# Kernel tuning notes

Measured on AMD Instinct MI355X. Metric: run time of the kernel, lower is better.

The kernel has to match this reference:

```python
import jax, jax.numpy as jnp
import numpy as np

N, E = 8000, 96000
S, V, G = 128, 64, 64          # scalar channels, l=1 vector channels, gate channels
LAT, OH = 128, 64
D = S + 3 * V                  # 320 feature dim per node/edge
AVG_NEIGH = 12.0
EPS = 1e-8

def _split(x):
    return x[:, :S], x[:, S:].reshape(x.shape[0], V, 3)

def sep_layernorm(x, ws, bs, wv):
    # separable LN: layernorm on l=0 scalars, component RMS norm on l=1 vectors
    s, v = _split(x)
    mu = jnp.mean(s, -1, keepdims=True)
    sc = s - mu
    s = sc * jax.lax.rsqrt(jnp.mean(sc * sc, -1, keepdims=True) + EPS) * ws + bs
    v = v * jax.lax.rsqrt(jnp.mean(v * v, (-2, -1), keepdims=True) + EPS) * wv[:, None]
    return s, v

def edge_frame(ev):
    # orthonormal frame with first axis along the edge (SO2 m=0 axis)
    a = ev * jax.lax.rsqrt(jnp.sum(ev * ev, -1, keepdims=True) + EPS)
    ref = jnp.where(jnp.abs(a[:, :1]) < 0.9,
                    jnp.array([1.0, 0.0, 0.0], ev.dtype),
                    jnp.array([0.0, 1.0, 0.0], ev.dtype))
    b = jnp.cross(a, ref)
    b = b * jax.lax.rsqrt(jnp.sum(b * b, -1, keepdims=True) + EPS)
    c = jnp.cross(a, b)
    return jnp.stack([a, b, c], axis=1)  # [E,3,3], rows are frame axes

def gate_act(s_all, v, n_s, n_g):
    s, g = s_all[:, :n_s], s_all[:, n_s:n_s + n_g]
    return jax.nn.silu(s), jax.nn.sigmoid(g)[:, :, None] * v

def e3_linear(s, v, ws, bs, wv):
    s = s @ ws * (1.0 / np.sqrt(s.shape[-1])) + bs
    v = jnp.einsum('eum,uk->ekm', v, wv) * (1.0 / np.sqrt(v.shape[1]))
    return s, v

def setup_inputs() -> dict:
    key = jax.random.key(0)
    ks = jax.random.split(key, 20)
    f = jnp.float32
    p = lambda k, sh: jax.random.normal(k, sh, f)
    inp = {}
    inp['latents'] = p(ks[0], (E, LAT))
    inp['node_features'] = p(ks[1], (N, D))
    inp['edge_features'] = p(ks[2], (E, D))
    at = jax.random.randint(ks[3], (N,), 0, OH)
    inp['atom_type'] = at
    inp['node_onehot'] = jax.nn.one_hot(at, OH, dtype=f)
    inp['edge_index'] = jax.random.randint(ks[4], (2, E), 0, N)
    inp['edge_vector'] = p(ks[5], (E, 3))
    inp['active_edges'] = jnp.arange(E)
    inp['sln_n_ws'] = jnp.ones((S,), f); inp['sln_n_bs'] = jnp.zeros((S,), f); inp['sln_n_wv'] = jnp.ones((V,), f)
    inp['sln_e_ws'] = jnp.ones((S,), f); inp['sln_e_bs'] = jnp.zeros((S,), f); inp['sln_e_wv'] = jnp.ones((V,), f)
    inp['so2_w0'] = p(ks[6], (3 * S + 3 * V, S + G + V))
    inp['so2_w1r'] = p(ks[7], (3 * V, V))
    inp['so2_w1i'] = p(ks[8], (3 * V, V))
    inp['env_w'] = p(ks[9], (LAT, S + V))
    inp['lp_ws'] = p(ks[10], (S, S)); inp['lp_bs'] = jnp.zeros((S,), f); inp['lp_wv'] = p(ks[11], (V, V))
    inp['oh_w_ss'] = p(ks[12], (S, OH, S))
    inp['oh_w_sg'] = p(ks[13], (S, OH, G))
    inp['oh_w_vv'] = p(ks[14], (V, OH, V))
    inp['ohl_ws'] = p(ks[15], (S, S)); inp['ohl_bs'] = jnp.zeros((S,), f); inp['ohl_wv'] = p(ks[16], (V, V))
    inp['res_param'] = jnp.zeros((1,), f)
    return inp

def reference(latents, node_features, edge_features, atom_type, node_onehot,
              edge_index, edge_vector, active_edges,
              sln_n_ws, sln_n_bs, sln_n_wv, sln_e_ws, sln_e_bs, sln_e_wv,
              so2_w0, so2_w1r, so2_w1i, env_w,
              lp_ws, lp_bs, lp_wv,
              oh_w_ss, oh_w_sg, oh_w_vv, ohl_ws, ohl_bs, ohl_wv, res_param):
    ctr = edge_index[0][active_edges]
    nbr = edge_index[1][active_edges]
    ns, nv = sep_layernorm(node_features, sln_n_ws, sln_n_bs, sln_n_wv)
    es, evf = sep_layernorm(edge_features, sln_e_ws, sln_e_bs, sln_e_wv)
    # concat center | edge | neighbor (scalars and vectors kept separate)
    sc = jnp.concatenate([ns[ctr], es, ns[nbr]], -1)          # [E, 3S]
    vc = jnp.concatenate([nv[ctr], evf, nv[nbr]], 1)          # [E, 3V, 3]
    R = edge_frame(edge_vector[active_edges])
    vf = jnp.einsum('eij,euj->eui', R, vc)                    # rotate into edge frame
    # SO2 linear: m=0 mixes scalars + on-axis components; m=+-1 mix with (re,im) weights
    m0_in = jnp.concatenate([sc, vf[:, :, 0]], -1)            # [E, 3S+3V]
    m0_out = m0_in @ so2_w0 * (1.0 / np.sqrt(m0_in.shape[-1]))  # [E, S+G+V]
    n1 = 1.0 / np.sqrt(vf.shape[1])
    vp = (vf[:, :, 1] @ so2_w1r - vf[:, :, 2] @ so2_w1i) * n1
    vm = (vf[:, :, 1] @ so2_w1i + vf[:, :, 2] @ so2_w1r) * n1
    v_out = jnp.stack([m0_out[:, S + G:], vp, vm], -1)        # [E,V,3] in frame
    v_out = jnp.einsum('eij,eui->euj', R, v_out)              # rotate back
    # gate activation + post linear
    ms, mv = gate_act(m0_out[:, :S + G], v_out, S, G)
    ms, mv = e3_linear(ms, mv, lp_ws, lp_bs, lp_wv)
    # env weighting (E3ElementLinear with weights from latents) + scatter to centers
    w = latents[active_edges] @ env_w * (1.0 / np.sqrt(LAT))  # [E, S+V]
    ms = ms * w[:, :S]
    mv = mv * w[:, S:, None]
    inv = 1.0 / np.sqrt(AVG_NEIGH)
    agg_s = jax.ops.segment_sum(ms, ctr, num_segments=N) * inv
    agg_v = jax.ops.segment_sum(mv, ctr, num_segments=N) * inv
    # one-hot FullyConnectedTensorProduct -> gate -> linear
    n_ss = 1.0 / np.sqrt(S * OH)
    n_vv = 1.0 / np.sqrt(V * OH)
    t_s = jnp.einsum('nu,nv,uvk->nk', agg_s, node_onehot, oh_w_ss) * n_ss
    t_g = jnp.einsum('nu,nv,uvk->nk', agg_s, node_onehot, oh_w_sg) * n_ss
    t_v = jnp.einsum('num,nv,uvk->nkm', agg_v, node_onehot, oh_w_vv) * n_vv
    gs, gv = gate_act(jnp.concatenate([t_s, t_g], -1), t_v, S, G)
    os_, ov = e3_linear(gs, gv, ohl_ws, ohl_bs, ohl_wv)
    new = jnp.concatenate([os_, ov.reshape(-1, 3 * V)], -1)
    # residual mixing (identity residual since node_irreps_in == irreps_out)
    alpha = jax.nn.sigmoid(res_param)[0]
    return alpha * node_features + (1.0 - alpha) * new
```

## Files before the change

### kernel.cpp

```cpp
#include <hip/hip_runtime.h>

#define EPS_LN 1e-8f

typedef __bf16 bf16x8 __attribute__((ext_vector_type(8)));
typedef float  f32x4  __attribute__((ext_vector_type(4)));

__device__ __forceinline__ float sigmoidf_(float x){ return 1.0f/(1.0f+__expf(-x)); }
__device__ __forceinline__ float siluf_(float x){ return x*sigmoidf_(x); }
__device__ __forceinline__ unsigned short f2bf(float x){ union{ __bf16 b; unsigned short u;} c; c.b = (__bf16)x; return c.u; }
__device__ __forceinline__ float bf2f(unsigned short u){ return __uint_as_float(((unsigned)u)<<16); }

union F4 { float4 v; float f[4]; };

__device__ __forceinline__ void st_bf4(char* base, int row, int stride_bytes, int k,
                                       float x0, float x1, float x2, float x3){
    union { __bf16 h[4]; unsigned long long u; } p;
    p.h[0]=(__bf16)x0; p.h[1]=(__bf16)x1; p.h[2]=(__bf16)x2; p.h[3]=(__bf16)x3;
    *(unsigned long long*)(base + row*stride_bytes + ((2*k) ^ ((row&7)<<4))) = p.u;
}
__device__ __forceinline__ bf16x8 ld_frag(const char* base, int row, int stride_bytes, int kbyte){
    return *(const bf16x8*)(base + row*stride_bytes + (kbyte ^ ((row&7)<<4)));
}
__device__ __forceinline__ void st_g4(__bf16* p, float x0, float x1, float x2, float x3){
    union { __bf16 h[4]; unsigned long long u; } pk;
// ... 26 lines not shown
                         const float* __restrict__ oh_vv,
                         __bf16* __restrict__ Wt, __bf16* __restrict__ w1rt, __bf16* __restrict__ w1it,
                         __bf16* __restrict__ Wevfm, __bf16* __restrict__ Bnodefm,
                         __bf16* __restrict__ Bvfm,
                         __bf16* __restrict__ envfm, __bf16* __restrict__ lpsfm,
                         __bf16* __restrict__ lpvfm,
                         __bf16* __restrict__ ssT, __bf16* __restrict__ sgT, __bf16* __restrict__ vvT)
{
    int t = blockIdx.x*256 + threadIdx.x;
    if (t < 576*256){
        int n = t/576, k = t%576;
        Wt[t] = (__bf16)w0[(size_t)k*256 + n];
    }
    if (t < 256*320){
        int n = t/320, k = t%320;
        int src = (k<128) ? (128+k) : (384+(k-128));
        Wevfm[fm_idx(n,k,10)] = (__bf16)w0[(size_t)src*256 + n];
    }
    if (t < 512*128){
        int n = t/128, k = t%128;
        float v = (n<256) ? w0[(size_t)k*256 + n] : w0[(size_t)(256+k)*256 + (n-256)];
        Bnodefm[fm_idx(n,k,4)] = (__bf16)v;
    }
    if (t < 64*192){
        int c = t/192, k = t%192;
        w1rt[t] = (__bf16)w1r[(size_t)k*64 + c];
        w1it[t] = (__bf16)w1i[(size_t)k*64 + c];
    }
    if (t < 128*384){
        int n = t/384, k = t%384;
        float v;
        if (n < 64) v = (k<192) ? w1r[(size_t)k*64+n] : -w1i[(size_t)(k-192)*64+n];
        else        v = (k<192) ? w1i[(size_t)k*64+(n-64)] : w1r[(size_t)(k-192)*64+(n-64)];
        Bvfm[fm_idx(n,k,12)] = (__bf16)v;
    }
    if (t < 192*128){ int n=t/128, k=t%128; envfm[fm_idx(n,k,4)] = (__bf16)env_w[(size_t)k*192+n]; }
    if (t < 128*128){ int n=t/128, k=t%128; lpsfm[fm_idx(n,k,4)] = (__bf16)lp_ws[(size_t)k*128+n]; }
    if (t < 64*64)  { int n=t/64,  k=t%64;  lpvfm[fm_idx(n,k,2)] = (__bf16)lp_wv[(size_t)k*64+n]; }
    if (t < 64*128*128){
        int at = t / 16384; int r = t & 16383; int u = r >> 7, k = r & 127;
        ssT[t] = (__bf16)oh_ss[((size_t)u*64 + at)*128 + k];
    }
    if (t < 64*128*64){
        int at = t / 8192; int r = t & 8191; int u = r >> 6, k = r & 63;
        sgT[t] = (__bf16)oh_sg[((size_t)u*64 + at)*64 + k];
    }
    if (t < 64*64*64){
        int at = t / 4096; int r = t & 4095; int u = r >> 6, k = r & 63;
        vvT[t] = (__bf16)oh_vv[((size_t)u*64 + at)*64 + k];
    }
}

__global__ void csr_count(const int* __restrict__ ei, const int* __restrict__ act,
                          int* __restrict__ cnt, int EA)
{
    int e = blockIdx.x*256 + threadIdx.x;
    if (e < EA) atomicAdd(&cnt[ei[act[e]]], 1);
}
__global__ void csr_scan(const int* __restrict__ cnt, int* __restrict__ offs,
                         int* __restrict__ cursor, int N)
{
    __shared__ int part[256];
    int t = threadIdx.x;
    int chunk = (N + 255) / 256;
    int lo = t*chunk, hi = lo+chunk; if (hi > N) hi = N; if (lo > N) lo = N;
    int s = 0;
    for (int i=lo;i<hi;i++) s += cnt[i];
    part[t] = s;
    __syncthreads();
    for (int d=1; d<256; d<<=1){
        int v = (t>=d) ? part[t-d] : 0;
        __syncthreads();
        part[t] += v;
        __syncthreads();
    }
    int run = (t==0) ? 0 : part[t-1];
    for (int i=lo;i<hi;i++){
        offs[i] = run; cursor[i] = run;
        run += cnt[i];
    }
    if (t==255) offs[N] = part[255];
}
__global__ void csr_fill(const int* __restrict__ ei, const int* __restrict__ act,
                         int* __restrict__ cursor, int* __restrict__ elist, int EA)
{
    int e = blockIdx.x*256 + threadIdx.x;
    if (e < EA){
        int n = ei[act[e]];
        int p = atomicAdd(&cursor[n], 1);
        elist[p] = e;
    }
}

__global__ void node_ln_kernel(const float* __restrict__ nf,
                               const float* __restrict__ ws, const float* __restrict__ bs,
                               const float* __restrict__ wv,
                               float* __restrict__ ns, float* __restrict__ nv,
                               __bf16* __restrict__ nsb, __bf16* __restrict__ nvb, int N)
{
    int t = threadIdx.x;
    int lane = t & 63;
    int n = blockIdx.x*4 + (t>>6);
    if (n >= N) return;
    const float* row = nf + (size_t)n*320;
    float s0 = row[lane], s1 = row[64+lane];
    float sum = s0+s1, sq = s0*s0+s1*s1;
    #pragma unroll
    for (int m=1;m<64;m<<=1){ sum += __shfl_xor(sum,m,64); sq += __shfl_xor(sq,m,64); }
    float mu = sum*(1.0f/128.0f);
    float rs = rsqrtf(sq*(1.0f/128.0f) - mu*mu + EPS_LN);
    float o0 = (s0-mu)*rs*ws[lane]    + bs[lane];
    float o1 = (s1-mu)*rs*ws[64+lane] + bs[64+lane];
    ns[(size_t)n*128+lane]    = o0;
    ns[(size_t)n*128+64+lane] = o1;
    nsb[(size_t)n*128+lane]    = (__bf16)o0;
    nsb[(size_t)n*128+64+lane] = (__bf16)o1;
    float v0 = row[128+lane], v1 = row[192+lane], v2 = row[256+lane];
    float vs = v0*v0+v1*v1+v2*v2;
    #pragma unroll
    for (int m=1;m<64;m<<=1) vs += __shfl_xor(vs,m,64);
    float rv = rsqrtf(vs*(1.0f/192.0f) + EPS_LN);
    float nv0 = v0*rv*wv[lane/3];
    float nv1 = v1*rv*wv[(64+lane)/3];
    float nv2 = v2*rv*wv[(128+lane)/3];
    nv[(size_t)n*192+lane]     = nv0;
    nv[(size_t)n*192+64+lane]  = nv1;
    nv[(size_t)n*192+128+lane] = nv2;
    nvb[(size_t)n*192+lane]     = (__bf16)nv0;
    nvb[(size_t)n*192+64+lane]  = (__bf16)nv1;
    nvb[(size_t)n*192+128+lane] = (__bf16)nv2;
}

__global__ void stage_kernel(
    const float* __restrict__ ef_all,
    const int*   __restrict__ edge_index,
    const float* __restrict__ edge_vector,
    const int*   __restrict__ active_edges,
    const float* __restrict__ e_ws, const float* __restrict__ e_bs, const float* __restrict__ e_wv,
    const __bf16* __restrict__ nvb,
    __bf16* __restrict__ m0in,
    __bf16* __restrict__ vfg,
    float* __restrict__ Rg, int2* __restrict__ ctnb,
    int EA, int EF)
{
    int tid = blockIdx.x*256 + threadIdx.x;
    int e = tid >> 4, l = tid & 15;
    if (e >= EA) return;
    int ae = active_edges[e];
    int ct = edge_index[ae];
    int nb = edge_index[EF + ae];
    float ex = edge_vector[(size_t)ae*3+0];
    float ey = edge_vector[(size_t)ae*3+1];
    float ez = edge_vector[(size_t)ae*3+2];
    float rn = rsqrtf(ex*ex+ey*ey+ez*ez + EPS_LN);
    float ax = ex*rn, ay = ey*rn, az = ez*rn;
    float rx, ry;
    if (fabsf(ax) < 0.9f) { rx = 1.0f; ry = 0.0f; } else { rx = 0.0f; ry = 1.0f; }
    float bx = -az*ry, by = az*rx, bz = ax*ry - ay*rx;
    float bn = rsqrtf(bx*bx+by*by+bz*bz + EPS_LN);
    bx*=bn; by*=bn; bz*=bn;
    float cx = ay*bz - az*by;
    float cy = az*bx - ax*bz;
    float cz = ax*by - ay*bx;
    if (l == 0){
        float* Rr = Rg + (size_t)e*12;
        *(float4*)(Rr)   = make_float4(ax,ay,az,bx);
        *(float4*)(Rr+4) = make_float4(by,bz,cx,cy);
        *(float4*)(Rr+8) = make_float4(cz,0.f,0.f,0.f);
        ctnb[e] = make_int2(ct, nb);
    }
    __bf16* Arow = m0in + (size_t)e*320;
    __bf16* V1r  = vfg + (size_t)e*384;
    __bf16* V2r  = V1r + 192;
    const float* ef = ef_all + (size_t)e*320;
    {
        F4 sa, sb;
        sa.v = *(const float4*)(ef + l*4);
        sb.v = *(const float4*)(ef + 64 + l*4);
        float sum=0.f, sq=0.f;
        #pragma unroll
        for (int i=0;i<4;i++){ sum += sa.f[i]+sb.f[i]; sq += sa.f[i]*sa.f[i]+sb.f[i]*sb.f[i]; }
        #pragma unroll
        for (int m=1;m<16;m<<=1){ sum += __shfl_xor(sum,m,64); sq += __shfl_xor(sq,m,64); }
        float mu = sum*(1.0f/128.0f);
        float rs = rsqrtf(sq*(1.0f/128.0f)-mu*mu + EPS_LN);
        float o0[4], o1[4];
        #pragma unroll
        for (int i=0;i<4;i++){
            int c0 = l*4+i, c1 = 64+l*4+i;
            o0[i] = (sa.f[i]-mu)*rs*e_ws[c0]+e_bs[c0];
            o1[i] = (sb.f[i]-mu)*rs*e_ws[c1]+e_bs[c1];
        }
        st_g4(Arow + l*4,      o0[0],o0[1],o0[2],o0[3]);
        st_g4(Arow + 64 + l*4, o1[0],o1[1],o1[2],o1[3]);
    }
    {
        F4 va, vb, vc;
        va.v = *(const float4*)(ef + 128 + l*12);
        vb.v = *(const float4*)(ef + 128 + l*12 + 4);
        vc.v = *(const float4*)(ef + 128 + l*12 + 8);
        float vv[12];
        #pragma unroll
        for (int i=0;i<4;i++){ vv[i]=va.f[i]; vv[4+i]=vb.f[i]; vv[8+i]=vc.f[i]; }
        float sq=0.f;
        #pragma unroll
        for (int i=0;i<12;i++) sq += vv[i]*vv[i];
        #pragma unroll
        for (int m=1;m<16;m<<=1) sq += __shfl_xor(sq,m,64);
        float rv = rsqrtf(sq*(1.0f/192.0f) + EPS_LN);
        float f0[4], f1[4], f2[4];
        #pragma unroll
        for (int j=0;j<4;j++){
            int u = 4*l + j;
            float sc = rv * e_wv[u];
            float x = vv[3*j]*sc, y = vv[3*j+1]*sc, z = vv[3*j+2]*sc;
            f0[j] = ax*x+ay*y+az*z;
            f1[j] = bx*x+by*y+bz*z;
            f2[j] = cx*x+cy*y+cz*z;
        }
        st_g4(Arow + 128 + 64 + 4*l, f0[0],f0[1],f0[2],f0[3]);
        st_g4(V1r + 64 + 4*l, f1[0],f1[1],f1[2],f1[3]);
        st_g4(V2r + 64 + 4*l, f2[0],f2[1],f2[2],f2[3]);
    }
    {
        float vv[12];
        ld_bf12(nvb + (size_t)ct*192 + l*12, vv);
        float f0[4], f1[4], f2[4];
        #pragma unroll
        for (int j=0;j<4;j++){
            float x = vv[3*j], y = vv[3*j+1], z = vv[3*j+2];
            f0[j] = ax*x+ay*y+az*z;
            f1[j] = bx*x+by*y+bz*z;
            f2[j] = cx*x+cy*y+cz*z;
        }
        st_g4(Arow + 128 + 4*l, f0[0],f0[1],f0[2],f0[3]);
        st_g4(V1r + 4*l, f1[0],f1[1],f1[2],f1[3]);
        st_g4(V2r + 4*l, f2[0],f2[1],f2[2],f2[3]);
    }
    {
        float vv[12];
        ld_bf12(nvb + (size_t)nb*192 + l*12, vv);
        float f0[4], f1[4], f2[4];
        #pragma unroll
        for (int j=0;j<4;j++){
            float x = vv[3*j], y = vv[3*j+1], z = vv[3*j+2];
            f0[j] = ax*x+ay*y+az*z;
            f1[j] = bx*x+by*y+bz*z;
            f2[j] = cx*x+cy*y+cz*z;
        }
        st_g4(Arow + 128 + 128 + 4*l, f0[0],f0[1],f0[2],f0[3]);
        st_g4(V1r + 128 + 4*l, f1[0],f1[1],f1[2],f1[3]);
        st_g4(V2r + 128 + 4*l, f2[0],f2[1],f2[2],f2[3]);
    }
}

enum { EPI_PLAIN=0, EPI_LPS=1, EPI_LPV=2 };

template<int N, int K, int RT, int EPI, bool AGATHER>
__global__ __launch_bounds__((N/64)*RT*64)
void gemm_k(const __bf16* __restrict__ Ag, const float* __restrict__ Agf,
            const int* __restrict__ aidx,
            const __bf16* __restrict__ Bfm,
            unsigned short* __restrict__ outp,
            const unsigned short* __restrict__ wenv,
            const float* __restrict__ bias,
            float scale, int M)
{
    constexpr int NT  = N/64;
    constexpr int BM  = RT*64;
    constexpr int T   = NT*RT*64;
    constexpr int NKT = K/32;
    constexpr int NK  = K/64;
    constexpr int NBUF= (NK>1) ? 2 : 1;
    constexpr int CA  = (BM*8 + T - 1)/T;
    __shared__ __align__(16) char lA[NBUF][BM*128];

    const int tid  = threadIdx.x;
    const int brow = blockIdx.x*BM;
    const int mpl  = blockIdx.y;
    const __bf16* A = AGATHER ? nullptr : (Ag + (size_t)mpl*M*K);

    uint4 ra[CA];
    auto loadA = [&](int ks){
        #pragma unroll
        for (int i=0;i<CA;i++){
            int c = tid + i*T;
            if (c < BM*8){
                int r = c>>3;
                int gr = brow + r; if (gr >= M) gr = M-1;
                if constexpr (AGATHER){
                    int ae = aidx[gr];
                    const float* base = Agf + (size_t)ae*K + ks*64 + (c&7)*8;
                    float4 f0 = *(const float4*)(base);
                    float4 f1 = *(const float4*)(base+4);
                    ra[i] = pack8(f0, f1);
                } else {
                    ra[i] = *(const uint4*)((const char*)(A + (size_t)gr*K + ks*64) + (c&7)*16);
                }
            }
        }
    };
    auto storeA = [&](int buf){
        #pragma unroll
        for (int i=0;i<CA;i++){
            int c = tid + i*T;
            if (c < BM*8){
                int r = c>>3, off = (c&7)*16;
                *(uint4*)(&lA[buf][r*128 + (off ^ ((r&7)<<4))]) = ra[i];
            }
        }
    };

    const int wid = tid>>6, ln = tid&63;
    const int cc = ln & 15, gq = ln >> 4;
    const int wn = wid % NT, wm = wid / NT;
    const __bf16* bbase = Bfm + ((size_t)wn*4*NKT)*512 + (size_t)ln*8;

    f32x4 acc[4][4];
    #pragma unroll
    for (int i=0;i<4;i++)
        #pragma unroll
        for (int j=0;j<4;j++) acc[i][j] = (f32x4){0,0,0,0};

    loadA(0); storeA(0);
    int cur = 0;
    for (int ks=0; ks<NK; ks++){
        __syncthreads();
        if (ks+1 < NK) loadA(ks+1);
        #pragma unroll
        for (int kt2=0;kt2<2;kt2++){
            const int kt = ks*2 + kt2;
            const int kb = kt2*64 + 16*gq;
            bf16x8 af[4];
            #pragma unroll
            for (int mf=0;mf<4;mf++){
                int r = wm*64 + mf*16 + cc;
                af[mf] = *(const bf16x8*)(&lA[cur][r*128 + (kb ^ ((r&7)<<4))]);
            }
            #pragma unroll
            for (int nf=0;nf<4;nf++){
                bf16x8 bfr = *(const bf16x8*)(bbase + ((size_t)nf*NKT + kt)*512);
                #pragma unroll
                for (int mf=0;mf<4;mf++)
                    acc[mf][nf] = __builtin_amdgcn_mfma_f32_16x16x32_bf16(af[mf], bfr, acc[mf][nf], 0,0,0);
            }
        }
        if (ks+1 < NK) storeA(cur^1);
        cur ^= (NBUF-1);
    }

    const float inv_avg_ = 0.288675134595f;
    #pragma unroll
    for (int mf=0;mf<4;mf++){
        #pragma unroll
        for (int nf=0;nf<4;nf++){
            #pragma unroll
            for (int j=0;j<4;j++){
                int gr = brow + wm*64 + mf*16 + gq*4 + j;
                if (gr >= M) continue;
                int col = wn*64 + nf*16 + cc;
                float v = acc[mf][nf][j];
                if constexpr (EPI == EPI_PLAIN){
                    outp[(size_t)gr*N + col] = f2bf(v*scale);
                } else if constexpr (EPI == EPI_LPS){
                    float val = (v*scale + bias[col]) * bf2f(wenv[(size_t)gr*192 + col]) * inv_avg_;
                    outp[(size_t)gr*320 + col] = f2bf(val);
                } else {
                    float val = v*0.125f * bf2f(wenv[(size_t)gr*192 + 128 + col]) * inv_avg_;
                    outp[(size_t)gr*320 + 128 + mpl*64 + col] = f2bf(val);
                }
            }
        }
    }
}

__global__ __launch_bounds__(128)
void gemm_lpv(const __bf16* __restrict__ Ag,
              const __bf16* __restrict__ Bfm,
              unsigned short* __restrict__ outp,
              const unsigned short* __restrict__ wenv,
              int M)
{
    constexpr int BM = 128;
    __shared__ __align__(16) char lA[BM*128];

    const int tid  = threadIdx.x;
    const int brow = blockIdx.x*BM;

    uint4 ra[8];
    auto loadA = [&](int pl){
        const __bf16* A = Ag + (size_t)pl*M*64;
        #pragma unroll
        for (int i=0;i<8;i++){
            int c = tid + i*128;
            int r = c>>3;
            int gr = brow + r; if (gr >= M) gr = M-1;
            ra[i] = *(const uint4*)((const char*)(A + (size_t)gr*64) + (c&7)*16);
        }
    };
    auto storeA = [&](){
        #pragma unroll
        for (int i=0;i<8;i++){
            int c = tid + i*128;
            int r = c>>3, off = (c&7)*16;
            *(uint4*)(&lA[r*128 + (off ^ ((r&7)<<4))]) = ra[i];
        }
    };

    const int wid = tid>>6, ln = tid&63;
    const int cc = ln & 15, gq = ln >> 4;
    const int wm = wid;

    bf16x8 bf_[4][2];
    {
        const __bf16* bbase = Bfm + (size_t)ln*8;
        #pragma unroll
        for (int nf=0;nf<4;nf++)
            #pragma unroll
            for (int kt=0;kt<2;kt++)
                bf_[nf][kt] = *(const bf16x8*)(bbase + ((size_t)nf*2 + kt)*512);
    }

    loadA(0); storeA();
    const float inv_avg_ = 0.288675134595f;
    for (int pl=0; pl<3; pl++){
        __syncthreads();
        if (pl < 2) loadA(pl+1);
        f32x4 acc[4][4];
        #pragma unroll
        for (int i=0;i<4;i++)
            #pragma unroll
            for (int j=0;j<4;j++) acc[i][j] = (f32x4){0,0,0,0};
        #pragma unroll
        for (int kt=0;kt<2;kt++){
            const int kb = kt*64 + 16*gq;
            bf16x8 af[4];
            #pragma unroll
            for (int mf=0;mf<4;mf++){
                int r = wm*64 + mf*16 + cc;
                af[mf] = *(const bf16x8*)(&lA[r*128 + (kb ^ ((r&7)<<4))]);
            }
            #pragma unroll
            for (int nf=0;nf<4;nf++)
                #pragma unroll
                for (int mf=0;mf<4;mf++)
                    acc[mf][nf] = __builtin_amdgcn_mfma_f32_16x16x32_bf16(af[mf], bf_[nf][kt], acc[mf][nf], 0,0,0);
        }
        __syncthreads();
        if (pl < 2) storeA();
        #pragma unroll
        for (int mf=0;mf<4;mf++){
            #pragma unroll
            for (int nf=0;nf<4;nf++){
                #pragma unroll
                for (int j=0;j<4;j++){
                    int gr = brow + wm*64 + mf*16 + gq*4 + j;
                    if (gr >= M) continue;
                    int col = nf*16 + cc;
                    float val = acc[mf][nf][j]*0.125f * bf2f(wenv[(size_t)gr*192 + 128 + col]) * inv_avg_;
                    outp[(size_t)gr*320 + 128 + pl*64 + col] = f2bf(val);
                }
            }
        }
    }
}

__global__ void mid_kernel(const unsigned short* __restrict__ m0out,
                           const unsigned short* __restrict__ vpvm,
                           const float* __restrict__ Rg,
                           const int2* __restrict__ ctnb,
                           const __bf16* __restrict__ nodeCN,
                           unsigned short* __restrict__ As,
                           unsigned short* __restrict__ MVp, int EA)
{
    int tid = blockIdx.x*256 + threadIdx.x;
    int e = tid>>6, u = tid&63;
    if (e >= EA) return;
    float rl = (u < 12) ? Rg[(size_t)e*12 + u] : 0.f;
    float R0=__shfl(rl,0,64), R1=__shfl(rl,1,64), R2=__shfl(rl,2,64);
    float R3=__shfl(rl,3,64), R4=__shfl(rl,4,64), R5=__shfl(rl,5,64);
    float R6=__shfl(rl,6,64), R7=__shfl(rl,7,64), R8=__shfl(rl,8,64);
    int2 cn = ctnb[e];
    const __bf16* nct = nodeCN + (size_t)cn.x*512;
    const __bf16* nnb = nodeCN + (size_t)cn.y*512 + 256;
    const float rn0 = 0.0416666666667f;
    float a0 = ((float)nct[u]       + (float)nnb[u])       * rn0;
    float a1 = ((float)nct[64+u]    + (float)nnb[64+u])    * rn0;
    float a2 = ((float)nct[128+u]   + (float)nnb[128+u])   * rn0;
    float a3 = ((float)nct[192+u]   + (float)nnb[192+u])   * rn0;
    const unsigned short* mo = m0out + (size_t)e*256;
    float m0 = bf2f(mo[u])       + a0;
    float m1 = bf2f(mo[64 + u])  + a1;
    float gt = sigmoidf_(bf2f(mo[128 + u]) + a2);
    float s0 = bf2f(mo[192 + u]) + a3;
    float p  = bf2f(vpvm[(size_t)e*128 + u]);
    float q  = bf2f(vpvm[(size_t)e*128 + 64 + u]);
    size_t eu = (size_t)e*64 + u;
    size_t P  = (size_t)EA*64;
    MVp[eu]       = f2bf(gt*(R0*s0 + R3*p + R6*q));
    MVp[P + eu]   = f2bf(gt*(R1*s0 + R4*p + R7*q));
    MVp[2*P + eu] = f2bf(gt*(R2*s0 + R5*p + R8*q));
    As[(size_t)e*128 + u]      = f2bf(siluf_(m0));
    As[(size_t)e*128 + 64 + u] = f2bf(siluf_(m1));
}

__launch_bounds__(256, 3)
__global__ void edge_kernel_fused(
    const float* __restrict__ latents,
    const float* __restrict__ ef_all,
    const int*   __restrict__ edge_index,
    const float* __restrict__ edge_vector,
    const int*   __restrict__ active_edges,
    const float* __restrict__ e_ws, const float* __restrict__ e_bs, const float* __restrict__ e_wv,
    const __bf16* __restrict__ Wt,
    const __bf16* __restrict__ w1rt,
    const __bf16* __restrict__ w1it,
    const float* __restrict__ env_w,
    const float* __restrict__ lp_ws, const float* __restrict__ lp_bs, const float* __restrict__ lp_wv,
    const float* __restrict__ ns, const float* __restrict__ nv,
    unsigned short* __restrict__ eout,
    int EA, int EF)
{
    __shared__ __align__(16) char smem[46592];
    char* sAbC = smem;
    char* sVFC = smem + 18432;
    float* sO  = (float*)smem;
    float* MV  = (float*)(smem + 16640);
    float* WE  = (float*)(smem + 33280);
    float* sR  = (float*)(smem + 45824);

    const int t = threadIdx.x;
    const int g = t >> 4, l = t & 15;
    const int e = blockIdx.x*16 + g;
    const bool act = (e < EA);

    int ct = 0, ae = 0;

    if (act) {
        ae = active_edges[e];
        ct = edge_index[ae];
        int nb = edge_index[EF + ae];
        float ex = edge_vector[(size_t)ae*3+0];
        float ey = edge_vector[(size_t)ae*3+1];
        float ez = edge_vector[(size_t)ae*3+2];
        float rn = rsqrtf(ex*ex+ey*ey+ez*ez + EPS_LN);
        float ax = ex*rn, ay = ey*rn, az = ez*rn;
        float rx, ry;
        if (fabsf(ax) < 0.9f) { rx = 1.0f; ry = 0.0f; } else { rx = 0.0f; ry = 1.0f; }
        float bx = -az*ry, by = az*rx, bz = ax*ry - ay*rx;
        float bn = rsqrtf(bx*bx+by*by+bz*bz + EPS_LN);
        bx*=bn; by*=bn; bz*=bn;
        float cx = ay*bz - az*by;
        float cy = az*bx - ax*bz;
        float cz = ax*by - ay*bx;
        if (l == 0){
            float* Rr = &sR[g*12];
            Rr[0]=ax; Rr[1]=ay; Rr[2]=az;
            Rr[3]=bx; Rr[4]=by; Rr[5]=bz;
            Rr[6]=cx; Rr[7]=cy; Rr[8]=cz;
        }
        {
            const float4* pc4 = (const float4*)(ns + (size_t)ct*128);
            const float4* pn4 = (const float4*)(ns + (size_t)nb*128);
            F4 a,b2,c,d;
            a.v = pc4[l]; b2.v = pc4[16+l]; c.v = pn4[l]; d.v = pn4[16+l];
            st_bf4(sAbC, g, 1152, l*4,       a.f[0],a.f[1],a.f[2],a.f[3]);
            st_bf4(sAbC, g, 1152, 64+l*4,    b2.f[0],b2.f[1],b2.f[2],b2.f[3]);
            st_bf4(sAbC, g, 1152, 256+l*4,   c.f[0],c.f[1],c.f[2],c.f[3]);
            st_bf4(sAbC, g, 1152, 320+l*4,   d.f[0],d.f[1],d.f[2],d.f[3]);
        }
        const float* ef = ef_all + (size_t)e*320;
        {
            F4 sa, sb;
            sa.v = *(const float4*)(ef + l*4);
            sb.v = *(const float4*)(ef + 64 + l*4);
            float sum=0.f, sq=0.f;
            #pragma unroll
            for (int i=0;i<4;i++){ sum += sa.f[i]+sb.f[i]; sq += sa.f[i]*sa.f[i]+sb.f[i]*sb.f[i]; }
            #pragma unroll
            for (int m=1;m<16;m<<=1){ sum += __shfl_xor(sum,m,64); sq += __shfl_xor(sq,m,64); }
            float mu = sum*(1.0f/128.0f);
            float rs = rsqrtf(sq*(1.0f/128.0f)-mu*mu + EPS_LN);
            float o0[4], o1[4];
            #pragma unroll
            for (int i=0;i<4;i++){
                int c0 = l*4+i, c1 = 64+l*4+i;
                o0[i] = (sa.f[i]-mu)*rs*e_ws[c0]+e_bs[c0];
                o1[i] = (sb.f[i]-mu)*rs*e_ws[c1]+e_bs[c1];
            }
            st_bf4(sAbC, g, 1152, 128+l*4, o0[0],o0[1],o0[2],o0[3]);
            st_bf4(sAbC, g, 1152, 192+l*4, o1[0],o1[1],o1[2],o1[3]);
        }
        {
            F4 va, vb, vc;
            va.v = *(const float4*)(ef + 128 + l*12);
            vb.v = *(const float4*)(ef + 128 + l*12 + 4);
            vc.v = *(const float4*)(ef + 128 + l*12 + 8);
            float vv[12];
            #pragma unroll
            for (int i=0;i<4;i++){ vv[i]=va.f[i]; vv[4+i]=vb.f[i]; vv[8+i]=vc.f[i]; }
            float sq=0.f;
            #pragma unroll
// ... 103 lines not shown
    __syncthreads();

    {
        const float rn0 = 0.0416666666667f;
        #pragma unroll
        for (int jt=0;jt<4;jt++){
            #pragma unroll
            for (int j=0;j<4;j++){
                sO[(gq*4+j)*260 + 64*w + 16*jt + cc] = accM[jt][j]*rn0;
            }
        }
    }
    float vp[4], vm[4];
    {
        const float n1 = 0.0721687836487f;
        #pragma unroll
        for (int j=0;j<4;j++){ vp[j] = (aP1[j]-aP2[j])*n1; vm[j] = (aM1[j]+aM2[j])*n1; }
    }
    __syncthreads();

    {
        int u = w*16 + cc;
        #pragma unroll
        for (int j=0;j<4;j++){
            int er = gq*4 + j;
            if (blockIdx.x*16 + er < EA){
                const float* Rr = &sR[er*12];
                float s0 = sO[er*260 + 192 + u];
                float gt = sigmoidf_(sO[er*260 + 128 + u]);
                float p = vp[j], q = vm[j];
                float4 o;
                o.x = gt*(Rr[0]*s0 + Rr[3]*p + Rr[6]*q);
                o.y = gt*(Rr[1]*s0 + Rr[4]*p + Rr[7]*q);
                o.z = gt*(Rr[2]*s0 + Rr[5]*p + Rr[8]*q);
                o.w = 0.0f;
                *(float4*)&MV[er*260 + u*4] = o;
            }
        }
    }
    if (act) {
        {
            int i0 = l*8;
            F4 oa, ob;
            oa.v = *(const float4*)&sO[g*260 + i0];
            ob.v = *(const float4*)&sO[g*260 + i0 + 4];
            #pragma unroll
            for (int i=0;i<4;i++){ oa.f[i] = siluf_(oa.f[i]); ob.f[i] = siluf_(ob.f[i]); }
            *(float4*)&sO[g*260 + i0]     = oa.v;
            *(float4*)&sO[g*260 + i0 + 4] = ob.v;
        }
        {
            const int cc2 = l*12;
            float wacc[12];
            #pragma unroll
            for (int i=0;i<12;i++) wacc[i]=0.f;
            const float* lat = latents + (size_t)ae*128;
            for (int k=0;k<128;k+=4){
                F4 la;
                la.v = *(const float4*)(lat + k);
                #pragma unroll
                for (int kk=0;kk<4;kk++){
                    const float* er_ = env_w + (size_t)(k+kk)*192 + cc2;
                    F4 e0v,e1v,e2v;
                    e0v.v = *(const float4*)(er_);
                    e1v.v = *(const float4*)(er_+4);
                    e2v.v = *(const float4*)(er_+8);
                    #pragma unroll
                    for (int i=0;i<4;i++){
                        wacc[i]   += la.f[kk]*e0v.f[i];
                        wacc[4+i] += la.f[kk]*e1v.f[i];
                        wacc[8+i] += la.f[kk]*e2v.f[i];
                    }
                }
            }
            const float inv128 = 0.0883883476483f;
            #pragma unroll
            for (int i=0;i<12;i++) WE[g*196 + cc2 + i] = wacc[i]*inv128;
        }
    }
    __syncthreads();

    if (act) {
        const float inv_avg = 0.288675134595f;
        unsigned short* orow = eout + (size_t)e*320;
        {
            int c0 = l*8;
            float a8[8];
            #pragma unroll
            for (int i=0;i<8;i++) a8[i]=0.f;
            for (int k=0;k<128;k+=4){
                F4 av;
                av.v = *(const float4*)&sO[g*260 + k];
                #pragma unroll
                for (int kk=0;kk<4;kk++){
                    const float* wr = lp_ws + (size_t)(k+kk)*128 + c0;
                    F4 w0, w1_;
                    w0.v  = *(const float4*)(wr);
                    w1_.v = *(const float4*)(wr+4);
                    #pragma unroll
                    for (int i=0;i<4;i++){ a8[i] += av.f[kk]*w0.f[i]; a8[4+i] += av.f[kk]*w1_.f[i]; }
                }
            }
            const float s128 = 0.0883883476483f;
            union { unsigned short h[8]; uint4 u; } ps;
            #pragma unroll
            for (int i=0;i<8;i++){
                int c = c0+i;
                ps.h[i] = f2bf((a8[i]*s128 + lp_bs[c]) * WE[g*196 + c] * inv_avg);
            }
            *(uint4*)(orow + c0) = ps.u;
        }
        {
            int k0 = l*4;
            float av[4][3];
            #pragma unroll
            for (int j=0;j<4;j++)
                #pragma unroll
                for (int m2=0;m2<3;m2++) av[j][m2]=0.f;
            for (int u=0;u<64;u++){
                F4 wv4, mv4;
                wv4.v = *(const float4*)(lp_wv + (size_t)u*64 + k0);
                mv4.v = *(const float4*)&MV[g*260 + u*4];
                #pragma unroll
                for (int j=0;j<4;j++){
                    av[j][0] += wv4.f[j]*mv4.f[0];
                    av[j][1] += wv4.f[j]*mv4.f[1];
                    av[j][2] += wv4.f[j]*mv4.f[2];
                }
            }
            #pragma unroll
            for (int j=0;j<4;j++){
                int k = k0+j;
                float wk = WE[g*196 + 128 + k] * 0.125f * inv_avg;
                orow[128 +       k] = f2bf(av[j][0]*wk);
                orow[128 + 64  + k] = f2bf(av[j][1]*wk);
                orow[128 + 128 + k] = f2bf(av[j][2]*wk);
            }
        }
    }
}

__global__ void node_out_kernel(
    const float* __restrict__ nf,
    const int* __restrict__ atom_type,
    const int* __restrict__ offs, const int* __restrict__ elist,
    const unsigned short* __restrict__ eout,
    const __bf16* __restrict__ ssT, const __bf16* __restrict__ sgT, const __bf16* __restrict__ vvT,
    const float* __restrict__ ohl_ws, const float* __restrict__ ohl_bs, const float* __restrict__ ohl_wv,
    const float* __restrict__ res_param,
    float* __restrict__ out, int N)
{
    __shared__ int   sE[64];
    __shared__ float AGS[128];
    __shared__ float AGV[192];
    __shared__ float TSs[128];
    __shared__ float SG[64];
    __shared__ float TV[192];
    __shared__ float PS[2560];
    const int n = blockIdx.x;
    const int t = threadIdx.x;
    const int at = atom_type[n];
    const int lo = offs[n], hi = offs[n+1];

    float aLo = 0.f, aHi = 0.f;
    for (int base = lo; base < hi; base += 64){
        int cnt = hi - base; if (cnt > 64) cnt = 64;
        __syncthreads();
        if (t < cnt) sE[t] = elist[base + t];
        __syncthreads();
        if (t < 160){
            int i = 0;
            for (; i+4 <= cnt; i += 4){
                unsigned x0 = *(const unsigned*)(eout + (size_t)sE[i  ]*320 + 2*t);
                unsigned x1 = *(const unsigned*)(eout + (size_t)sE[i+1]*320 + 2*t);
                unsigned x2 = *(const unsigned*)(eout + (size_t)sE[i+2]*320 + 2*t);
                unsigned x3 = *(const unsigned*)(eout + (size_t)sE[i+3]*320 + 2*t);
                aLo += bf2f((unsigned short)x0) + bf2f((unsigned short)x1)
                     + bf2f((unsigned short)x2) + bf2f((unsigned short)x3);
                aHi += bf2f((unsigned short)(x0>>16)) + bf2f((unsigned short)(x1>>16))
                     + bf2f((unsigned short)(x2>>16)) + bf2f((unsigned short)(x3>>16));
            }
            for (; i < cnt; i++){
                unsigned x = *(const unsigned*)(eout + (size_t)sE[i]*320 + 2*t);
                aLo += bf2f((unsigned short)x);
                aHi += bf2f((unsigned short)(x>>16));
            }
        }
    }
    if (t < 160){
        int c0 = 2*t, c1 = 2*t+1;
        if (c0 < 128) AGS[c0] = aLo; else { int d=c0-128; AGV[(d&63)*3 + (d>>6)] = aLo; }
        if (c1 < 128) AGS[c1] = aHi; else { int d=c1-128; AGV[(d&63)*3 + (d>>6)] = aHi; }
    }
    __syncthreads();
    const float n_ss = 0.0110485434560f;
    const float n_vv = 0.015625f;

    {
        int us = t >> 6, kp = t & 63;
        float aclo = 0.f, achi = 0.f;
        const __bf16* w = ssT + (size_t)at*16384 + 2*kp;
        #pragma unroll 4
        for (int u = us; u < 128; u += 4){
            unsigned w2 = *(const unsigned*)(w + (size_t)u*128);
            float a = AGS[u];
            aclo += a * bf2f((unsigned short)w2);
            achi += a * bf2f((unsigned short)(w2>>16));
        }
        PS[us*128 + 2*kp]   = aclo;
        PS[us*128 + 2*kp+1] = achi;
    }
    {
        int us = t >> 5, kp = t & 31;
        float aclo = 0.f, achi = 0.f;
        const __bf16* w = sgT + (size_t)at*8192 + 2*kp;
        #pragma unroll 4
        for (int u = us; u < 128; u += 8){
            unsigned w2 = *(const unsigned*)(w + (size_t)u*64);
            float a = AGS[u];
            aclo += a * bf2f((unsigned short)w2);
            achi += a * bf2f((unsigned short)(w2>>16));
        }
        PS[512 + us*64 + 2*kp]   = aclo;
        PS[512 + us*64 + 2*kp+1] = achi;
    }
    {
        int us = t >> 5, kp = t & 31;
        float ac00=0,ac01=0,ac02=0, ac10=0,ac11=0,ac12=0;
        const __bf16* w = vvT + (size_t)at*4096 + 2*kp;
        #pragma unroll 2
        for (int u = us; u < 64; u += 8){
            unsigned w2 = *(const unsigned*)(w + (size_t)u*64);
            float w0 = bf2f((unsigned short)w2), w1 = bf2f((unsigned short)(w2>>16));
            float a0 = AGV[u*3+0], a1 = AGV[u*3+1], a2 = AGV[u*3+2];
            ac00 += a0*w0; ac01 += a1*w0; ac02 += a2*w0;
            ac10 += a0*w1; ac11 += a1*w1; ac12 += a2*w1;
        }
        float* pv = &PS[1024 + us*192];
        pv[(2*kp)*3+0]=ac00; pv[(2*kp)*3+1]=ac01; pv[(2*kp)*3+2]=ac02;
        pv[(2*kp+1)*3+0]=ac10; pv[(2*kp+1)*3+1]=ac11; pv[(2*kp+1)*3+2]=ac12;
    }
    __syncthreads();
    if (t < 128){
        float s = PS[t] + PS[128+t] + PS[256+t] + PS[384+t];
        TSs[t] = siluf_(s*n_ss);
    } else if (t < 192){
        int k = t-128;
        float s = 0.f;
        #pragma unroll
        for (int us=0; us<8; us++) s += PS[512 + us*64 + k];
        SG[k] = sigmoidf_(s*n_ss);
    } else {
        int k = t-192;
        float s0=0,s1=0,s2=0;
        #pragma unroll
        for (int us=0; us<8; us++){
            const float* pv = &PS[1024 + us*192 + k*3];
            s0 += pv[0]; s1 += pv[1]; s2 += pv[2];
        }
        TV[k*3+0]=s0*n_vv; TV[k*3+1]=s1*n_vv; TV[k*3+2]=s2*n_vv;
    }
    __syncthreads();
    const float alpha = sigmoidf_(res_param[0]);
    const float beta  = 1.0f - alpha;
    if (t < 128) {
        float acc = 0.0f;
        #pragma unroll 8
        for (int k=0;k<128;k++) acc += TSs[k]*ohl_ws[(size_t)k*128 + t];
        float val = acc*0.0883883476483f + ohl_bs[t];
        out[(size_t)n*320 + t] = alpha*nf[(size_t)n*320 + t] + beta*val;
    } else if (t >= 192) {
        int k = t-192;
        float a0=0,a1=0,a2=0;
        #pragma unroll 8
        for (int u=0;u<64;u++){
            float w = ohl_wv[(size_t)u*64 + k]*SG[u];
            a0 += TV[u*3+0]*w; a1 += TV[u*3+1]*w; a2 += TV[u*3+2]*w;
        }
        size_t base = (size_t)n*320 + 128 + (size_t)k*3;
        out[base+0] = alpha*nf[base+0] + beta*(a0*0.125f);
        out[base+1] = alpha*nf[base+1] + beta*(a1*0.125f);
        out[base+2] = alpha*nf[base+2] + beta*(a2*0.125f);
    }
}

extern "C" void kernel_launch(void* const* d_in, const int* in_sizes, int n_in,
                              void* d_out, int out_size, void* d_ws, size_t ws_size,
                              hipStream_t stream)
{
    const float* latents       = (const float*)d_in[0];
    const float* node_features = (const float*)d_in[1];
    const float* edge_features = (const float*)d_in[2];
    const int*   atom_type     = (const int*)d_in[3];
    const int*   edge_index    = (const int*)d_in[5];
    const float* edge_vector   = (const float*)d_in[6];
    const int*   active_edges  = (const int*)d_in[7];
    const float* sln_n_ws = (const float*)d_in[8];
    const float* sln_n_bs = (const float*)d_in[9];
    const float* sln_n_wv = (const float*)d_in[10];
    const float* sln_e_ws = (const float*)d_in[11];
    const float* sln_e_bs = (const float*)d_in[12];
    const float* sln_e_wv = (const float*)d_in[13];
    const float* so2_w0   = (const float*)d_in[14];
    const float* so2_w1r  = (const float*)d_in[15];
    const float* so2_w1i  = (const float*)d_in[16];
    const float* env_w    = (const float*)d_in[17];
    const float* lp_ws    = (const float*)d_in[18];
    const float* lp_bs    = (const float*)d_in[19];
    const float* lp_wv    = (const float*)d_in[20];
    const float* oh_w_ss  = (const float*)d_in[21];
    const float* oh_w_sg  = (const float*)d_in[22];
    const float* oh_w_vv  = (const float*)d_in[23];
    const float* ohl_ws   = (const float*)d_in[24];
    const float* ohl_bs   = (const float*)d_in[25];
    const float* ohl_wv   = (const float*)d_in[26];
    const float* res_param= (const float*)d_in[27];
    float* out = (float*)d_out;

    const int N  = in_sizes[1] / 320;
    const int EF = in_sizes[5] / 2;
    const int EA = in_sizes[7];

    char* p = (char*)d_ws;
    auto alloc = [&](size_t bytes) -> char* {
        char* r = p; p += (bytes + 255) & ~(size_t)255; return r;
    };
    float* ns      = (float*)alloc((size_t)N*128*4);
    float* nv      = (float*)alloc((size_t)N*192*4);
    __bf16* nsb    = (__bf16*)alloc((size_t)N*128*2);
    __bf16* nvb    = (__bf16*)alloc((size_t)N*192*2);
    int*   cnt     = (int*)  alloc((size_t)N*4);
    int*   offs    = (int*)  alloc(((size_t)N+1)*4);
    int*   cursor  = (int*)  alloc((size_t)N*4);
    int*   elist   = (int*)  alloc((size_t)EA*4);
    __bf16* Wt     = (__bf16*)alloc((size_t)576*256*2);
    __bf16* w1rt   = (__bf16*)alloc((size_t)64*192*2);
    __bf16* w1it   = (__bf16*)alloc((size_t)64*192*2);
    __bf16* Wevfm  = (__bf16*)alloc((size_t)256*320*2);
    __bf16* Bnodefm= (__bf16*)alloc((size_t)512*128*2);
    __bf16* Bvfm   = (__bf16*)alloc((size_t)128*384*2);
    __bf16* envfm  = (__bf16*)alloc((size_t)192*128*2);
    __bf16* lpsfm  = (__bf16*)alloc((size_t)128*128*2);
    __bf16* lpvfm  = (__bf16*)alloc((size_t)64*64*2);
    __bf16* ssT    = (__bf16*)alloc((size_t)64*128*128*2);
    __bf16* sgT    = (__bf16*)alloc((size_t)64*128*64*2);
    __bf16* vvT    = (__bf16*)alloc((size_t)64*64*64*2);
    __bf16* nodeCN = (__bf16*)alloc((size_t)N*512*2);
    int2*  ctnb    = (int2*) alloc((size_t)EA*8);
    unsigned short* eout = (unsigned short*)alloc((size_t)EA*320*2);
    unsigned short* w_env= (unsigned short*)alloc((size_t)EA*192*2);
    float*  Rg    = (float*) alloc((size_t)EA*12*4);
    __bf16* m0in  = (__bf16*)alloc((size_t)EA*320*2);
    __bf16* vfg   = (__bf16*)alloc((size_t)EA*384*2);
    size_t split_need = (size_t)(p - (char*)d_ws);
    const bool use_split = (split_need <= ws_size);

    unsigned short* vpvm  = eout;
    unsigned short* m0out = (unsigned short*)vfg;
    unsigned short* As    = (unsigned short*)m0in;
    unsigned short* MVp   = As + (size_t)EA*128;

    hipMemsetAsync(cnt, 0, (size_t)N*sizeof(int), stream);
    prep_all<<<4096, 256, 0, stream>>>(so2_w0, so2_w1r, so2_w1i, env_w, lp_ws, lp_wv,
                                       oh_w_ss, oh_w_sg, oh_w_vv,
                                       Wt, w1rt, w1it, Wevfm, Bnodefm, Bvfm,
                                       envfm, lpsfm, lpvfm, ssT, sgT, vvT);
    node_ln_kernel<<<(N+3)/4, 256, 0, stream>>>(node_features, sln_n_ws, sln_n_bs, sln_n_wv, ns, nv, nsb, nvb, N);
    csr_count<<<(EA+255)/256, 256, 0, stream>>>(edge_index, active_edges, cnt, EA);
    csr_scan<<<1, 256, 0, stream>>>(cnt, offs, cursor, N);
    csr_fill<<<(EA+255)/256, 256, 0, stream>>>(edge_index, active_edges, cursor, elist, EA);

    const float rn0    = 0.0416666666667f;
    const float n1     = 0.0721687836487f;
    const float inv128 = 0.0883883476483f;

    if (use_split){
        const int NB64  = (EA + 63) / 64;
        const int NB128 = (EA + 127) / 128;
        const int NBn   = (N + 63) / 64;
        gemm_k<512,128,1,EPI_PLAIN,false><<<dim3(NBn,1), 512, 0, stream>>>(
            nsb, nullptr, nullptr, Bnodefm, (unsigned short*)nodeCN, nullptr, nullptr, 1.0f, N);
        stage_kernel<<<(EA+15)/16, 256, 0, stream>>>(edge_features, edge_index, edge_vector, active_edges,
            sln_e_ws, sln_e_bs, sln_e_wv, nvb, m0in, vfg, Rg, ctnb, EA, EF);
        gemm_k<128,384,2,EPI_PLAIN,false><<<dim3(NB128,1), 256, 0, stream>>>(
            vfg, nullptr, nullptr, Bvfm, vpvm, nullptr, nullptr, n1, EA);
        gemm_k<256,320,1,EPI_PLAIN,false><<<dim3(NB64,1), 256, 0, stream>>>(
            m0in, nullptr, nullptr, Wevfm, m0out, nullptr, nullptr, rn0, EA);
        mid_kernel<<<(EA*64+255)/256, 256, 0, stream>>>(m0out, vpvm, Rg, ctnb, nodeCN, As, MVp, EA);
        gemm_k<192,128,1,EPI_PLAIN,true><<<dim3(NB64,1), 192, 0, stream>>>(
            nullptr, latents, active_edges, envfm, w_env, nullptr, nullptr, inv128, EA);
        gemm_k<128,128,2,EPI_LPS,false><<<dim3(NB128,1), 256, 0, stream>>>(
            (const __bf16*)As, nullptr, nullptr, lpsfm, eout, w_env, lp_bs, inv128, EA);
        gemm_lpv<<<NB128, 128, 0, stream>>>(
            (const __bf16*)MVp, lpvfm, eout, w_env, EA);
    } else {
        edge_kernel_fused<<<(EA+15)/16, 256, 0, stream>>>(latents, edge_features, edge_index, edge_vector, active_edges,
            sln_e_ws, sln_e_bs, sln_e_wv, Wt, w1rt, w1it, env_w, lp_ws, lp_bs, lp_wv,
            ns, nv, eout, EA, EF);
    }
    node_out_kernel<<<N, 256, 0, stream>>>(node_features, atom_type, offs, elist, eout,
        ssT, sgT, vvT, ohl_ws, ohl_bs, ohl_wv, res_param, out, N);
}
```

Before: 443.7 us.

## Scatter edge outputs into CSR-sorted order so node reduction reads contiguously

csr_fill now records each edge's slot in the center-sorted order instead of building an edge list. The final GEMM epilogues and the fused edge kernel write each edge's output row to that sorted slot. node_out_kernel can then sum a contiguous block of rows without an indirection through shared memory and block-wide syncs. This trades coalesced GEMM epilogue stores for scattered row writes, in exchange for contiguous reads in the segment sum.

```diff
diff --git a/kernel.cpp b/kernel.cpp
--- a/kernel.cpp
+++ b/kernel.cpp
@@ -132,13 +132,13 @@
     if (t==255) offs[N] = part[255];
 }
 __global__ void csr_fill(const int* __restrict__ ei, const int* __restrict__ act,
-                         int* __restrict__ cursor, int* __restrict__ elist, int EA)
+                         int* __restrict__ cursor, int* __restrict__ pos, int EA)
 {
     int e = blockIdx.x*256 + threadIdx.x;
     if (e < EA){
         int n = ei[act[e]];
         int p = atomicAdd(&cursor[n], 1);
-        elist[p] = e;
+        pos[e] = p;
     }
 }
 
@@ -304,7 +304,7 @@
     }
 }
 
-enum { EPI_PLAIN=0, EPI_LPS=1, EPI_LPV=2 };
+enum { EPI_PLAIN=0, EPI_LPS=1 };
 
 template<int N, int K, int RT, int EPI, bool AGATHER>
 __global__ __launch_bounds__((N/64)*RT*64)
@@ -314,6 +314,7 @@
             unsigned short* __restrict__ outp,
             const unsigned short* __restrict__ wenv,
             const float* __restrict__ bias,
+            const int* __restrict__ pos,
             float scale, int M)
 {
     constexpr int NT  = N/64;
@@ -412,12 +413,9 @@
                 float v = acc[mf][nf][j];
                 if constexpr (EPI == EPI_PLAIN){
                     outp[(size_t)gr*N + col] = f2bf(v*scale);
-                } else if constexpr (EPI == EPI_LPS){
+                } else {
                     float val = (v*scale + bias[col]) * bf2f(wenv[(size_t)gr*192 + col]) * inv_avg_;
-                    outp[(size_t)gr*320 + col] = f2bf(val);
-                } else {
-                    float val = v*0.125f * bf2f(wenv[(size_t)gr*192 + 128 + col]) * inv_avg_;
-                    outp[(size_t)gr*320 + 128 + mpl*64 + col] = f2bf(val);
+                    outp[(size_t)pos[gr]*320 + col] = f2bf(val);
                 }
             }
         }
@@ -429,6 +427,7 @@
               const __bf16* __restrict__ Bfm,
               unsigned short* __restrict__ outp,
               const unsigned short* __restrict__ wenv,
+              const int* __restrict__ pos,
               int M)
 {
     constexpr int BM = 128;
@@ -508,7 +507,7 @@
                     if (gr >= M) continue;
                     int col = nf*16 + cc;
                     float val = acc[mf][nf][j]*0.125f * bf2f(wenv[(size_t)gr*192 + 128 + col]) * inv_avg_;
-                    outp[(size_t)gr*320 + 128 + pl*64 + col] = f2bf(val);
+                    outp[(size_t)pos[gr]*320 + 128 + pl*64 + col] = f2bf(val);
                 }
             }
         }
@@ -568,6 +567,7 @@
     const float* __restrict__ env_w,
     const float* __restrict__ lp_ws, const float* __restrict__ lp_bs, const float* __restrict__ lp_wv,
     const float* __restrict__ ns, const float* __restrict__ nv,
+    const int* __restrict__ pos,
     unsigned short* __restrict__ eout,
     int EA, int EF)
 {
@@ -837,7 +837,7 @@
 
     if (act) {
         const float inv_avg = 0.288675134595f;
-        unsigned short* orow = eout + (size_t)e*320;
+        unsigned short* orow = eout + (size_t)pos[e]*320;
         {
             int c0 = l*8;
             float a8[8];
@@ -898,14 +898,13 @@
 __global__ void node_out_kernel(
     const float* __restrict__ nf,
     const int* __restrict__ atom_type,
-    const int* __restrict__ offs, const int* __restrict__ elist,
+    const int* __restrict__ offs,
     const unsigned short* __restrict__ eout,
     const __bf16* __restrict__ ssT, const __bf16* __restrict__ sgT, const __bf16* __restrict__ vvT,
     const float* __restrict__ ohl_ws, const float* __restrict__ ohl_bs, const float* __restrict__ ohl_wv,
     const float* __restrict__ res_param,
     float* __restrict__ out, int N)
 {
-    __shared__ int   sE[64];
     __shared__ float AGS[128];
     __shared__ float AGV[192];
     __shared__ float TSs[128];
@@ -917,32 +916,26 @@
     const int at = atom_type[n];
     const int lo = offs[n], hi = offs[n+1];
 
-    float aLo = 0.f, aHi = 0.f;
-    for (int base = lo; base < hi; base += 64){
-        int cnt = hi - base; if (cnt > 64) cnt = 64;
-        __syncthreads();
-        if (t < cnt) sE[t] = elist[base + t];
-        __syncthreads();
-        if (t < 160){
-            int i = 0;
-            for (; i+4 <= cnt; i += 4){
-                unsigned x0 = *(const unsigned*)(eout + (size_t)sE[i  ]*320 + 2*t);
-                unsigned x1 = *(const unsigned*)(eout + (size_t)sE[i+1]*320 + 2*t);
-                unsigned x2 = *(const unsigned*)(eout + (size_t)sE[i+2]*320 + 2*t);
-                unsigned x3 = *(const unsigned*)(eout + (size_t)sE[i+3]*320 + 2*t);
-                aLo += bf2f((unsigned short)x0) + bf2f((unsigned short)x1)
-                     + bf2f((unsigned short)x2) + bf2f((unsigned short)x3);
-                aHi += bf2f((unsigned short)(x0>>16)) + bf2f((unsigned short)(x1>>16))
-                     + bf2f((unsigned short)(x2>>16)) + bf2f((unsigned short)(x3>>16));
-            }
-            for (; i < cnt; i++){
-                unsigned x = *(const unsigned*)(eout + (size_t)sE[i]*320 + 2*t);
-                aLo += bf2f((unsigned short)x);
-                aHi += bf2f((unsigned short)(x>>16));
-            }
-        }
-    }
     if (t < 160){
+        float aLo = 0.f, aHi = 0.f;
+        const unsigned short* base = eout + (size_t)lo*320 + 2*t;
+        int cnt = hi - lo;
+        int i = 0;
+        for (; i+4 <= cnt; i += 4){
+            unsigned x0 = *(const unsigned*)(base + (size_t)(i  )*320);
+            unsigned x1 = *(const unsigned*)(base + (size_t)(i+1)*320);
+            unsigned x2 = *(const unsigned*)(base + (size_t)(i+2)*320);
+            unsigned x3 = *(const unsigned*)(base + (size_t)(i+3)*320);
+            aLo += bf2f((unsigned short)x0) + bf2f((unsigned short)x1)
+                 + bf2f((unsigned short)x2) + bf2f((unsigned short)x3);
+            aHi += bf2f((unsigned short)(x0>>16)) + bf2f((unsigned short)(x1>>16))
+                 + bf2f((unsigned short)(x2>>16)) + bf2f((unsigned short)(x3>>16));
+        }
+        for (; i < cnt; i++){
+            unsigned x = *(const unsigned*)(base + (size_t)i*320);
+            aLo += bf2f((unsigned short)x);
+            aHi += bf2f((unsigned short)(x>>16));
+        }
         int c0 = 2*t, c1 = 2*t+1;
         if (c0 < 128) AGS[c0] = aLo; else { int d=c0-128; AGV[(d&63)*3 + (d>>6)] = aLo; }
         if (c1 < 128) AGS[c1] = aHi; else { int d=c1-128; AGV[(d&63)*3 + (d>>6)] = aHi; }
@@ -1087,7 +1080,7 @@
     int*   cnt     = (int*)  alloc((size_t)N*4);
     int*   offs    = (int*)  alloc(((size_t)N+1)*4);
     int*   cursor  = (int*)  alloc((size_t)N*4);
-    int*   elist   = (int*)  alloc((size_t)EA*4);
+    int*   pos     = (int*)  alloc((size_t)EA*4);
     __bf16* Wt     = (__bf16*)alloc((size_t)576*256*2);
     __bf16* w1rt   = (__bf16*)alloc((size_t)64*192*2);
     __bf16* w1it   = (__bf16*)alloc((size_t)64*192*2);
@@ -1123,7 +1116,7 @@
     node_ln_kernel<<<(N+3)/4, 256, 0, stream>>>(node_features, sln_n_ws, sln_n_bs, sln_n_wv, ns, nv, nsb, nvb, N);
     csr_count<<<(EA+255)/256, 256, 0, stream>>>(edge_index, active_edges, cnt, EA);
     csr_scan<<<1, 256, 0, stream>>>(cnt, offs, cursor, N);
-    csr_fill<<<(EA+255)/256, 256, 0, stream>>>(edge_index, active_edges, cursor, elist, EA);
+    csr_fill<<<(EA+255)/256, 256, 0, stream>>>(edge_index, active_edges, cursor, pos, EA);
 
     const float rn0    = 0.0416666666667f;
     const float n1     = 0.0721687836487f;
@@ -1134,25 +1127,25 @@
         const int NB128 = (EA + 127) / 128;
         const int NBn   = (N + 63) / 64;
         gemm_k<512,128,1,EPI_PLAIN,false><<<dim3(NBn,1), 512, 0, stream>>>(
-            nsb, nullptr, nullptr, Bnodefm, (unsigned short*)nodeCN, nullptr, nullptr, 1.0f, N);
+            nsb, nullptr, nullptr, Bnodefm, (unsigned short*)nodeCN, nullptr, nullptr, nullptr, 1.0f, N);
         stage_kernel<<<(EA+15)/16, 256, 0, stream>>>(edge_features, edge_index, edge_vector, active_edges,
             sln_e_ws, sln_e_bs, sln_e_wv, nvb, m0in, vfg, Rg, ctnb, EA, EF);
         gemm_k<128,384,2,EPI_PLAIN,false><<<dim3(NB128,1), 256, 0, stream>>>(
-            vfg, nullptr, nullptr, Bvfm, vpvm, nullptr, nullptr, n1, EA);
+            vfg, nullptr, nullptr, Bvfm, vpvm, nullptr, nullptr, nullptr, n1, EA);
         gemm_k<256,320,1,EPI_PLAIN,false><<<dim3(NB64,1), 256, 0, stream>>>(
-            m0in, nullptr, nullptr, Wevfm, m0out, nullptr, nullptr, rn0, EA);
+            m0in, nullptr, nullptr, Wevfm, m0out, nullptr, nullptr, nullptr, rn0, EA);
         mid_kernel<<<(EA*64+255)/256, 256, 0, stream>>>(m0out, vpvm, Rg, ctnb, nodeCN, As, MVp, EA);
         gemm_k<192,128,1,EPI_PLAIN,true><<<dim3(NB64,1), 192, 0, stream>>>(
-            nullptr, latents, active_edges, envfm, w_env, nullptr, nullptr, inv128, EA);
+            nullptr, latents, active_edges, envfm, w_env, nullptr, nullptr, nullptr, inv128, EA);
         gemm_k<128,128,2,EPI_LPS,false><<<dim3(NB128,1), 256, 0, stream>>>(
-            (const __bf16*)As, nullptr, nullptr, lpsfm, eout, w_env, lp_bs, inv128, EA);
+            (const __bf16*)As, nullptr, nullptr, lpsfm, eout, w_env, lp_bs, pos, inv128, EA);
         gemm_lpv<<<NB128, 128, 0, stream>>>(
-            (const __bf16*)MVp, lpvfm, eout, w_env, EA);
+            (const __bf16*)MVp, lpvfm, eout, w_env, pos, EA);
     } else {
         edge_kernel_fused<<<(EA+15)/16, 256, 0, stream>>>(latents, edge_features, edge_index, edge_vector, active_edges,
             sln_e_ws, sln_e_bs, sln_e_wv, Wt, w1rt, w1it, env_w, lp_ws, lp_bs, lp_wv,
-            ns, nv, eout, EA, EF);
-    }
-    node_out_kernel<<<N, 256, 0, stream>>>(node_features, atom_type, offs, elist, eout,
+            ns, nv, pos, eout, EA, EF);
+    }
+    node_out_kernel<<<N, 256, 0, stream>>>(node_features, atom_type, offs, eout,
         ssT, sgT, vvT, ohl_ws, ohl_bs, ohl_wv, res_param, out, N);
 }
```

Measured after the change: 446.6 us. Within noise of the previous version (+0.6%).
